# Performance work log

Measured on AMD Instinct MI355X. Metric: run time of the kernel, lower is better.

The kernel has to match this reference:

```python
import jax, jax.numpy as jnp
import numpy as np

N_NODES = 8192
N_EDGES = 16384
IN_CH = 32
HID = 64
OUT_CH = 2
EDGE_DIM = 4
N_LAYERS = 3
N_GRAPHS = 256
BN_EPS = 1e-5


def setup_inputs() -> dict:
    key = jax.random.key(0)
    ks = jax.random.split(key, 16)
    x = jax.random.normal(ks[0], (N_NODES, IN_CH), dtype=jnp.float32)
    edge_index = jax.random.randint(ks[1], (2, N_EDGES), 0, N_NODES, dtype=jnp.int32)
    edge_attr = jax.random.uniform(ks[2], (N_EDGES, EDGE_DIM), dtype=jnp.float32)
    batch = jnp.sort(jax.random.randint(ks[3], (N_NODES,), 0, N_GRAPHS, dtype=jnp.int32))
    s = 0.05
    params = {
        'lin_in_W': jax.random.normal(ks[4], (IN_CH, HID), jnp.float32) * s,
        'lin_in_b': jnp.zeros((HID,), jnp.float32),
        'edge_W': jax.random.normal(ks[5], (N_LAYERS, EDGE_DIM, HID * HID), jnp.float32) * s,
        'edge_b': jax.random.normal(ks[6], (N_LAYERS, HID * HID), jnp.float32) * s,
        'root_W': jax.random.normal(ks[7], (N_LAYERS, HID, HID), jnp.float32) * s,
        'conv_b': jnp.zeros((N_LAYERS, HID), jnp.float32),
        'bn_gamma': jnp.ones((N_LAYERS, HID), jnp.float32),
        'bn_beta': jnp.zeros((N_LAYERS, HID), jnp.float32),
        'bn_mean': jax.random.normal(ks[8], (N_LAYERS, HID), jnp.float32) * s,
        'bn_var': jax.random.uniform(ks[9], (N_LAYERS, HID), jnp.float32, 0.5, 1.5),
        'clf_W': jax.random.normal(ks[10], (HID, OUT_CH), jnp.float32) * s,
        'clf_b': jnp.zeros((OUT_CH,), jnp.float32),
    }
    return {'x': x, 'edge_index': edge_index, 'edge_attr': edge_attr, 'batch': batch, **params}


def reference(x, edge_index, edge_attr, batch, lin_in_W, lin_in_b, edge_W, edge_b,
              root_W, conv_b, bn_gamma, bn_beta, bn_mean, bn_var, clf_W, clf_b):
    # lin_in
    h = x @ lin_in_W + lin_in_b  # [N, H]
    src, dst = edge_index[0], edge_index[1]  # PyG: row0 = source j, row1 = target i
    for l in range(N_LAYERS):
        # edge network: per-edge weight matrix [E, H, H]
        W_e = (edge_attr @ edge_W[l] + edge_b[l]).reshape(N_EDGES, HID, HID)
        # message: gather x_j, per-edge matmul
        msg = jnp.einsum('eh,eho->eo', h[src], W_e)  # [E, H]
        # scatter-add aggregation at target nodes
        agg = jax.ops.segment_sum(msg, dst, num_segments=N_NODES)  # [N, H]
        # NNConv update: root transform + bias
        h = agg + h @ root_W[l] + conv_b[l]
        # BatchNorm1d (inference: running stats), then ReLU (dropout off in eval)
        h = (h - bn_mean[l]) * jax.lax.rsqrt(bn_var[l] + BN_EPS) * bn_gamma[l] + bn_beta[l]
        h = jax.nn.relu(h)
    # global_add_pool over graph ids
    pooled = jax.ops.segment_sum(h, batch, num_segments=N_GRAPHS)  # [G, H]
    return pooled @ clf_W + clf_b  # [G, OUT_CH]
```

## Files before the change

### kernel.cpp

```cpp
#include <hip/hip_runtime.h>

#define N_NODES 8192
#define N_EDGES 16384
#define IN_CH 32
#define HID 64
#define EDGE_DIM 4
#define N_LAYERS 3
#define N_GRAPHS 256
#define BN_EPS 1e-5f

#define NT 512
#define NPB 16
#define NBLK (N_NODES / NPB)
#define ECAP 96

__global__ void kzero(float4* __restrict__ p, int n4) {
    int i = blockIdx.x * blockDim.x + threadIdx.x;
    if (i < n4) p[i] = make_float4(0.f, 0.f, 0.f, 0.f);
}

__global__ __launch_bounds__(NT, 4) void k0(
        const float* __restrict__ x,
        const float* __restrict__ Win, const float* __restrict__ bin,
        const float* __restrict__ eW, const float* __restrict__ eB,
        const int* __restrict__ ei, const float* __restrict__ ea,
        float* __restrict__ hG, float* __restrict__ aggA,
        float* __restrict__ aggB, float* __restrict__ pooled,
        int* __restrict__ gbcnt, int2* __restrict__ gsd, float4* __restrict__ gea) {
    __shared__ float  Wis[IN_CH * HID];
    __shared__ float  xs[NPB * IN_CH];
    __shared__ float  hs[NPB * HID];
    __shared__ float  ys[NPB * 5 * HID];
    __shared__ int    cntE;
    __shared__ int2   eSL[ECAP];
    __shared__ float4 eEA[ECAP];

    const int t = threadIdx.x, b = blockIdx.x, node0 = b * NPB;
    const int c = t & 63, g = t >> 6;

    for (int i = t; i < NPB * HID; i += NT) aggB[node0 * HID + i] = 0.f;
    {
        int gi = b * NT + t;
        if (gi < N_GRAPHS * HID) pooled[gi] = 0.f;
    }
    if (t == 0) cntE = 0;
    for (int i = t; i < IN_CH * HID; i += NT) Wis[i] = Win[i];
    for (int i = t; i < NPB * IN_CH; i += NT) xs[i] = x[node0 * IN_CH + i];
    __syncthreads();

    {
        float bb = bin[c];
        float h0 = bb, h1 = bb;
        const float* x0 = xs + (2 * g + 0) * IN_CH;
        const float* x1 = xs + (2 * g + 1) * IN_CH;
#pragma unroll
        for (int k = 0; k < IN_CH; ++k) {
            float wk = Wis[k * HID + c];
            h0 += x0[k] * wk; h1 += x1[k] * wk;
        }
        hs[(2 * g + 0) * HID + c] = h0; hG[(node0 + 2 * g + 0) * HID + c] = h0;
        hs[(2 * g + 1) * HID + c] = h1; hG[(node0 + 2 * g + 1) * HID + c] = h1;
    }

    {
        float acc[2][5] = {};
#pragma unroll 4
        for (int k = 0; k < HID; ++k) {
            float w0 = eW[0 * 4096 + k * 64 + c];
            float w1 = eW[1 * 4096 + k * 64 + c];
            float w2 = eW[2 * 4096 + k * 64 + c];
            float w3 = eW[3 * 4096 + k * 64 + c];
            float w4 = eB[k * 64 + c];
            float a0 = hs[(2 * g + 0) * HID + k];
            float a1 = hs[(2 * g + 1) * HID + k];
            acc[0][0] += a0 * w0; acc[0][1] += a0 * w1; acc[0][2] += a0 * w2;
            acc[0][3] += a0 * w3; acc[0][4] += a0 * w4;
            acc[1][0] += a1 * w0; acc[1][1] += a1 * w1; acc[1][2] += a1 * w2;
            acc[1][3] += a1 * w3; acc[1][4] += a1 * w4;
        }
#pragma unroll
        for (int j = 0; j < 2; ++j)
#pragma unroll
            for (int d = 0; d < 5; ++d)
                ys[(2 * g + j) * (5 * HID) + d * HID + c] = acc[j][d];
    }

    for (int e = t; e < N_EDGES; e += NT) {
        int src = ei[e];
        if ((src >> 4) == b) {
            int slot = atomicAdd(&cntE, 1);
            if (slot < ECAP) {
                int2 sd = make_int2(src & 15, ei[N_EDGES + e]);
                float4 a4 = *(const float4*)(ea + 4 * (size_t)e);
                eSL[slot] = sd;           eEA[slot] = a4;
                gsd[b * ECAP + slot] = sd; gea[b * ECAP + slot] = a4;
            }
        }
    }
    __syncthreads();
    int cnt = min(cntE, ECAP);
    if (t == 0) gbcnt[b] = cnt;

    for (int e = g; e < cnt; e += 8) {
        int2 sd = eSL[e];
        float4 a = eEA[e];
        const float* yr = ys + sd.x * (5 * HID);
        float m = a.x * yr[c] + a.y * yr[HID + c] + a.z * yr[2 * HID + c] +
                  a.w * yr[3 * HID + c] + yr[4 * HID + c];
        atomicAdd(&aggA[sd.y * HID + c], m);
    }
}

template <int ZERO_IN, int LAST>
__global__ __launch_bounds__(NT, 4) void klayer(
        float* __restrict__ hG,
        float* __restrict__ aggIn, float* __restrict__ aggOut,
        const float* __restrict__ rootW, const float* __restrict__ conv_b,
        const float* __restrict__ gam, const float* __restrict__ bet,
        const float* __restrict__ mu, const float* __restrict__ var,
        const float* __restrict__ eW, const float* __restrict__ eB,
        const int* __restrict__ gbcnt, const int2* __restrict__ gsd,
        const float4* __restrict__ gea,
        const int* __restrict__ batch, float* __restrict__ pooled) {
    __shared__ float  Ws[HID * HID];
    __shared__ float  hsin[NPB * HID];
    __shared__ float  ys[NPB * 5 * HID];
    __shared__ int2   eSL[ECAP];
    __shared__ float4 eEA[ECAP];

    const int t = threadIdx.x, b = blockIdx.x, node0 = b * NPB;
    const int c = t & 63, g = t >> 6;

    int cnt = LAST ? 0 : min(gbcnt[b], ECAP);
    for (int i = t; i < HID * HID; i += NT) Ws[i] = rootW[i];
    for (int i = t; i < NPB * HID; i += NT) hsin[i] = hG[node0 * HID + i];
    if (!LAST) {
        for (int i = t; i < cnt; i += NT) { eSL[i] = gsd[b * ECAP + i]; eEA[i] = gea[b * ECAP + i]; }
    }
    __syncthreads();

    float scale = gam[c] * rsqrtf(var[c] + BN_EPS);
    float shift = bet[c] - mu[c] * scale;
    float cb = conv_b[c];

    float hnew[2];
#pragma unroll
    for (int j = 0; j < 2; ++j) {
        int ln = 2 * g + j, n = node0 + ln;
        float acc = 0.f;
        const float4* hv = (const float4*)(hsin + ln * HID);
#pragma unroll
        for (int k4 = 0; k4 < HID / 4; ++k4) {
            float4 h4 = hv[k4];
            acc += h4.x * Ws[(4 * k4 + 0) * 64 + c] + h4.y * Ws[(4 * k4 + 1) * 64 + c] +
                   h4.z * Ws[(4 * k4 + 2) * 64 + c] + h4.w * Ws[(4 * k4 + 3) * 64 + c];
        }
        float av = aggIn[n * HID + c];
        if (ZERO_IN) aggIn[n * HID + c] = 0.f;
        hnew[j] = fmaxf((av + acc + cb) * scale + shift, 0.f);
    }
    hsin[(2 * g + 0) * HID + c] = hnew[0];
    hsin[(2 * g + 1) * HID + c] = hnew[1];

    if (!LAST) {
        hG[(node0 + 2 * g + 0) * HID + c] = hnew[0];
        hG[(node0 + 2 * g + 1) * HID + c] = hnew[1];
        float acc[2][5] = {};
#pragma unroll 4
        for (int k = 0; k < HID; ++k) {
            float w0 = eW[0 * 4096 + k * 64 + c];
            float w1 = eW[1 * 4096 + k * 64 + c];
            float w2 = eW[2 * 4096 + k * 64 + c];
            float w3 = eW[3 * 4096 + k * 64 + c];
            float w4 = eB[k * 64 + c];
            float a0 = hsin[(2 * g + 0) * HID + k];
            float a1 = hsin[(2 * g + 1) * HID + k];
            acc[0][0] += a0 * w0; acc[0][1] += a0 * w1; acc[0][2] += a0 * w2;
            acc[0][3] += a0 * w3; acc[0][4] += a0 * w4;
            acc[1][0] += a1 * w0; acc[1][1] += a1 * w1; acc[1][2] += a1 * w2;
            acc[1][3] += a1 * w3; acc[1][4] += a1 * w4;
        }
#pragma unroll
        for (int j = 0; j < 2; ++j)
#pragma unroll
            for (int d = 0; d < 5; ++d)
                ys[(2 * g + j) * (5 * HID) + d * HID + c] = acc[j][d];
        __syncthreads();

        for (int e = g; e < cnt; e += 8) {
            int2 sd = eSL[e];
            float4 a = eEA[e];
            const float* yr = ys + sd.x * (5 * HID);
            float m = a.x * yr[c] + a.y * yr[HID + c] + a.z * yr[2 * HID + c] +
                      a.w * yr[3 * HID + c] + yr[4 * HID + c];
            atomicAdd(&aggOut[sd.y * HID + c], m);
        }
    } else {
        int n0 = node0 + 2 * g, n1 = n0 + 1;
        atomicAdd(&pooled[batch[n0] * HID + c], hnew[0]);
        atomicAdd(&pooled[batch[n1] * HID + c], hnew[1]);
    }
}

__global__ void kclf(const float* __restrict__ pooled,
                     const float* __restrict__ W,
                     const float* __restrict__ bb,
                     float* __restrict__ out) {
    int lane = threadIdx.x & 63;
    int gph = blockIdx.x * 4 + (threadIdx.x >> 6);
    float p = pooled[gph * HID + lane];
    float2 w = ((const float2*)W)[lane];
    float r0 = p * w.x, r1 = p * w.y;
#pragma unroll
    for (int off = 32; off; off >>= 1) {
        r0 += __shfl_xor(r0, off, 64);
        r1 += __shfl_xor(r1, off, 64);
    }
    if (lane == 0) {
        out[gph * 2 + 0] = r0 + bb[0];
        out[gph * 2 + 1] = r1 + bb[1];
    }
}

extern "C" void kernel_launch(void* const* d_in, const int* in_sizes, int n_in,
                              void* d_out, int out_size, void* d_ws, size_t ws_size,
                              hipStream_t stream) {
    const float* x         = (const float*)d_in[0];
    const int*   edge_index= (const int*)  d_in[1];
    const float* edge_attr = (const float*)d_in[2];
    const int*   batch     = (const int*)  d_in[3];
    const float* lin_in_W  = (const float*)d_in[4];
    const float* lin_in_b  = (const float*)d_in[5];
    const float* edge_W    = (const float*)d_in[6];
    const float* edge_b    = (const float*)d_in[7];
    const float* root_W    = (const float*)d_in[8];
    const float* conv_b    = (const float*)d_in[9];
    const float* bn_gamma  = (const float*)d_in[10];
    const float* bn_beta   = (const float*)d_in[11];
    const float* bn_mean   = (const float*)d_in[12];
    const float* bn_var    = (const float*)d_in[13];
    const float* clf_W     = (const float*)d_in[14];
    const float* clf_b     = (const float*)d_in[15];
    float* out = (float*)d_out;

    char* ws = (char*)d_ws;
    float*  aggA   = (float*) (ws);
    float*  aggB   = (float*) (ws + (size_t)2 * 1024 * 1024);
    float*  pooled = (float*) (ws + (size_t)4 * 1024 * 1024);
    int*    gbcnt  = (int*)   (ws + (size_t)4 * 1024 * 1024 + 65536);
    float*  hG     = (float*) (ws + (size_t)5 * 1024 * 1024);
    int2*   gsd    = (int2*)  (ws + (size_t)7 * 1024 * 1024);
    float4* gea    = (float4*)(ws + (size_t)7 * 1024 * 1024 + 512 * 1024);

    const int n4 = (2 * 1024 * 1024) / 16;
    kzero<<<(n4 + 255) / 256, 256, 0, stream>>>((float4*)aggA, n4);

    k0<<<NBLK, NT, 0, stream>>>(x, lin_in_W, lin_in_b, edge_W, edge_b,
                                edge_index, edge_attr, hG, aggA, aggB, pooled,
                                gbcnt, gsd, gea);

    klayer<1, 0><<<NBLK, NT, 0, stream>>>(
        hG, aggA, aggB, root_W, conv_b, bn_gamma, bn_beta, bn_mean, bn_var,
        edge_W + (size_t)1 * EDGE_DIM * HID * HID, edge_b + (size_t)1 * HID * HID,
        gbcnt, gsd, gea, batch, pooled);

    klayer<0, 0><<<NBLK, NT, 0, stream>>>(
        hG, aggB, aggA, root_W + (size_t)1 * HID * HID, conv_b + (size_t)1 * HID,
        bn_gamma + HID, bn_beta + HID, bn_mean + HID, bn_var + HID,
        edge_W + (size_t)2 * EDGE_DIM * HID * HID, edge_b + (size_t)2 * HID * HID,
        gbcnt, gsd, gea, batch, pooled);

    klayer<0, 1><<<NBLK, NT, 0, stream>>>(
        hG, aggA, aggB, root_W + (size_t)2 * HID * HID, conv_b + (size_t)2 * HID,
        bn_gamma + 2 * HID, bn_beta + 2 * HID, bn_mean + 2 * HID, bn_var + 2 * HID,
        edge_W, edge_b,
        gbcnt, gsd, gea, batch, pooled);

    kclf<<<N_GRAPHS / 4, 256, 0, stream>>>(pooled, clf_W, clf_b, out);
}
```

Before: 72.35 us.

## Pre-transpose weights to float4 layout, bin edges per node, fuse classifier into last layer

A prep kernel repacks lin_in, root and edge-network weights into a k4-interleaved float4 layout, zeroes the aggregation buffer and seeds the output with the classifier bias, replacing the zero kernel. Edges are binned per source node in registers-friendly per-node lists, so message values are computed directly from per-thread accumulators instead of staging a shared ys table and syncing. Root weights are read from global/L2 instead of being copied to shared memory, cutting LDS use and a barrier. The pooling plus classifier are fused into the last layer via wave reductions and atomics on the output, dropping the pooled buffer and kclf launch. Per-node cap of 20 edges could drop edges if a node has high out-degree.

```diff
diff --git a/kernel.cpp b/kernel.cpp
--- a/kernel.cpp
+++ b/kernel.cpp
@@ -12,102 +12,137 @@
 #define NT 512
 #define NPB 16
 #define NBLK (N_NODES / NPB)
-#define ECAP 96
-
-__global__ void kzero(float4* __restrict__ p, int n4) {
-    int i = blockIdx.x * blockDim.x + threadIdx.x;
-    if (i < n4) p[i] = make_float4(0.f, 0.f, 0.f, 0.f);
+#define NCAP 20
+
+#define WT_ROOT(l) (512 + (l) * 1024)
+#define WT_E(l) (3584 + (l) * 5120)
+#define WT_F4 18944
+
+__global__ __launch_bounds__(256) void kprep(
+        const float* __restrict__ Win, const float* __restrict__ rootW,
+        const float* __restrict__ eW, const float* __restrict__ eB,
+        const float* __restrict__ clf_b,
+        float4* __restrict__ WT4, float4* __restrict__ aggA4,
+        float* __restrict__ out) {
+    int i = blockIdx.x * 256 + threadIdx.x;
+    aggA4[i] = make_float4(0.f, 0.f, 0.f, 0.f);
+    if (i < N_GRAPHS * 2) out[i] = clf_b[i & 1];
+    if (i < WT_F4) {
+        const float* base;
+        int k4, c;
+        if (i < 512) {
+            k4 = i >> 6; c = i & 63; base = Win;
+        } else if (i < 3584) {
+            int oo = i - 512; int l = oo >> 10; int r = oo & 1023;
+            k4 = r >> 6; c = r & 63; base = rootW + l * 4096;
+        } else {
+            int oo = i - 3584; int l = oo / 5120; int r = oo % 5120;
+            int d = r >> 10; int rr = r & 1023;
+            k4 = rr >> 6; c = rr & 63;
+            base = (d < 4) ? (eW + (size_t)l * 16384 + d * 4096)
+                           : (eB + (size_t)l * 4096);
+        }
+        float4 v;
+        v.x = base[(k4 * 4 + 0) * 64 + c];
+        v.y = base[(k4 * 4 + 1) * 64 + c];
+        v.z = base[(k4 * 4 + 2) * 64 + c];
+        v.w = base[(k4 * 4 + 3) * 64 + c];
+        WT4[i] = v;
+    }
 }
 
 __global__ __launch_bounds__(NT, 4) void k0(
-        const float* __restrict__ x,
-        const float* __restrict__ Win, const float* __restrict__ bin,
-        const float* __restrict__ eW, const float* __restrict__ eB,
+        const float* __restrict__ x, const float* __restrict__ bin,
+        const float4* __restrict__ WT4,
         const int* __restrict__ ei, const float* __restrict__ ea,
-        float* __restrict__ hG, float* __restrict__ aggA,
-        float* __restrict__ aggB, float* __restrict__ pooled,
-        int* __restrict__ gbcnt, int2* __restrict__ gsd, float4* __restrict__ gea) {
-    __shared__ float  Wis[IN_CH * HID];
+        float* __restrict__ hG, float* __restrict__ aggA, float* __restrict__ aggB,
+        int* __restrict__ gcnt, int* __restrict__ gdst, float4* __restrict__ gea4) {
     __shared__ float  xs[NPB * IN_CH];
     __shared__ float  hs[NPB * HID];
-    __shared__ float  ys[NPB * 5 * HID];
-    __shared__ int    cntE;
-    __shared__ int2   eSL[ECAP];
-    __shared__ float4 eEA[ECAP];
+    __shared__ int    cntN[NPB];
+    __shared__ int    eDL[NPB * NCAP];
+    __shared__ float4 eEA[NPB * NCAP];
 
     const int t = threadIdx.x, b = blockIdx.x, node0 = b * NPB;
     const int c = t & 63, g = t >> 6;
 
-    for (int i = t; i < NPB * HID; i += NT) aggB[node0 * HID + i] = 0.f;
+    if (t < 256) ((float4*)(aggB + node0 * HID))[t] = make_float4(0.f, 0.f, 0.f, 0.f);
+    if (t < NPB) cntN[t] = 0;
     {
-        int gi = b * NT + t;
-        if (gi < N_GRAPHS * HID) pooled[gi] = 0.f;
-    }
-    if (t == 0) cntE = 0;
-    for (int i = t; i < IN_CH * HID; i += NT) Wis[i] = Win[i];
-    for (int i = t; i < NPB * IN_CH; i += NT) xs[i] = x[node0 * IN_CH + i];
+        int ln = 2 * g + (c >> 5);
+        xs[ln * IN_CH + (c & 31)] = x[(node0 + ln) * IN_CH + (c & 31)];
+    }
     __syncthreads();
+
+    const int4* src4 = (const int4*)ei;
+    for (int e4 = t; e4 < N_EDGES / 4; e4 += NT) {
+        int4 s4 = src4[e4];
+        int ss[4] = {s4.x, s4.y, s4.z, s4.w};
+#pragma unroll
+        for (int q = 0; q < 4; ++q) {
+            if ((ss[q] >> 4) == b) {
+                int local = ss[q] & 15;
+                int slot = atomicAdd(&cntN[local], 1);
+                if (slot < NCAP) {
+                    int e = e4 * 4 + q;
+                    int dst = ei[N_EDGES + e];
+                    float4 a4 = *(const float4*)(ea + 4 * (size_t)e);
+                    eDL[local * NCAP + slot] = dst;
+                    eEA[local * NCAP + slot] = a4;
+                    gdst[(node0 + local) * NCAP + slot] = dst;
+                    gea4[(node0 + local) * NCAP + slot] = a4;
+                }
+            }
+        }
+    }
 
     {
         float bb = bin[c];
         float h0 = bb, h1 = bb;
-        const float* x0 = xs + (2 * g + 0) * IN_CH;
-        const float* x1 = xs + (2 * g + 1) * IN_CH;
-#pragma unroll
-        for (int k = 0; k < IN_CH; ++k) {
-            float wk = Wis[k * HID + c];
-            h0 += x0[k] * wk; h1 += x1[k] * wk;
+        const float4* x0 = (const float4*)(xs + (2 * g + 0) * IN_CH);
+        const float4* x1 = (const float4*)(xs + (2 * g + 1) * IN_CH);
+#pragma unroll
+        for (int k4 = 0; k4 < IN_CH / 4; ++k4) {
+            float4 w = WT4[k4 * 64 + c];
+            float4 a = x0[k4], d = x1[k4];
+            h0 += a.x * w.x + a.y * w.y + a.z * w.z + a.w * w.w;
+            h1 += d.x * w.x + d.y * w.y + d.z * w.z + d.w * w.w;
         }
         hs[(2 * g + 0) * HID + c] = h0; hG[(node0 + 2 * g + 0) * HID + c] = h0;
         hs[(2 * g + 1) * HID + c] = h1; hG[(node0 + 2 * g + 1) * HID + c] = h1;
     }
 
+    float acc[2][5] = {};
     {
-        float acc[2][5] = {};
+        const float4* E = WT4 + WT_E(0);
+        const float4* h0v = (const float4*)(hs + (2 * g + 0) * HID);
+        const float4* h1v = (const float4*)(hs + (2 * g + 1) * HID);
 #pragma unroll 4
-        for (int k = 0; k < HID; ++k) {
-            float w0 = eW[0 * 4096 + k * 64 + c];
-            float w1 = eW[1 * 4096 + k * 64 + c];
-            float w2 = eW[2 * 4096 + k * 64 + c];
-            float w3 = eW[3 * 4096 + k * 64 + c];
-            float w4 = eB[k * 64 + c];
-            float a0 = hs[(2 * g + 0) * HID + k];
-            float a1 = hs[(2 * g + 1) * HID + k];
-            acc[0][0] += a0 * w0; acc[0][1] += a0 * w1; acc[0][2] += a0 * w2;
-            acc[0][3] += a0 * w3; acc[0][4] += a0 * w4;
-            acc[1][0] += a1 * w0; acc[1][1] += a1 * w1; acc[1][2] += a1 * w2;
-            acc[1][3] += a1 * w3; acc[1][4] += a1 * w4;
-        }
-#pragma unroll
-        for (int j = 0; j < 2; ++j)
-#pragma unroll
-            for (int d = 0; d < 5; ++d)
-                ys[(2 * g + j) * (5 * HID) + d * HID + c] = acc[j][d];
-    }
-
-    for (int e = t; e < N_EDGES; e += NT) {
-        int src = ei[e];
-        if ((src >> 4) == b) {
-            int slot = atomicAdd(&cntE, 1);
-            if (slot < ECAP) {
-                int2 sd = make_int2(src & 15, ei[N_EDGES + e]);
-                float4 a4 = *(const float4*)(ea + 4 * (size_t)e);
-                eSL[slot] = sd;           eEA[slot] = a4;
-                gsd[b * ECAP + slot] = sd; gea[b * ECAP + slot] = a4;
+        for (int k4 = 0; k4 < 16; ++k4) {
+            float4 a = h0v[k4], d = h1v[k4];
+#pragma unroll
+            for (int dd = 0; dd < 5; ++dd) {
+                float4 w = E[(dd * 16 + k4) * 64 + c];
+                acc[0][dd] += a.x * w.x + a.y * w.y + a.z * w.z + a.w * w.w;
+                acc[1][dd] += d.x * w.x + d.y * w.y + d.z * w.z + d.w * w.w;
             }
         }
     }
     __syncthreads();
-    int cnt = min(cntE, ECAP);
-    if (t == 0) gbcnt[b] = cnt;
-
-    for (int e = g; e < cnt; e += 8) {
-        int2 sd = eSL[e];
-        float4 a = eEA[e];
-        const float* yr = ys + sd.x * (5 * HID);
-        float m = a.x * yr[c] + a.y * yr[HID + c] + a.z * yr[2 * HID + c] +
-                  a.w * yr[3 * HID + c] + yr[4 * HID + c];
-        atomicAdd(&aggA[sd.y * HID + c], m);
+
+    if (t < NPB) gcnt[node0 + t] = min(cntN[t], NCAP);
+
+#pragma unroll
+    for (int j = 0; j < 2; ++j) {
+        int ln = 2 * g + j;
+        int cd = min(cntN[ln], NCAP);
+        for (int s = 0; s < cd; ++s) {
+            int dst = eDL[ln * NCAP + s];
+            float4 a = eEA[ln * NCAP + s];
+            float m = a.x * acc[j][0] + a.y * acc[j][1] + a.z * acc[j][2] +
+                      a.w * acc[j][3] + acc[j][4];
+            atomicAdd(&aggA[dst * HID + c], m);
+        }
     }
 }
 
@@ -115,45 +150,38 @@
 __global__ __launch_bounds__(NT, 4) void klayer(
         float* __restrict__ hG,
         float* __restrict__ aggIn, float* __restrict__ aggOut,
-        const float* __restrict__ rootW, const float* __restrict__ conv_b,
+        const float4* __restrict__ WT4, int lidx,
+        const float* __restrict__ conv_b,
         const float* __restrict__ gam, const float* __restrict__ bet,
         const float* __restrict__ mu, const float* __restrict__ var,
-        const float* __restrict__ eW, const float* __restrict__ eB,
-        const int* __restrict__ gbcnt, const int2* __restrict__ gsd,
-        const float4* __restrict__ gea,
-        const int* __restrict__ batch, float* __restrict__ pooled) {
-    __shared__ float  Ws[HID * HID];
-    __shared__ float  hsin[NPB * HID];
-    __shared__ float  ys[NPB * 5 * HID];
-    __shared__ int2   eSL[ECAP];
-    __shared__ float4 eEA[ECAP];
+        const int* __restrict__ gcnt, const int* __restrict__ gdst,
+        const float4* __restrict__ gea4,
+        const int* __restrict__ batch, const float* __restrict__ clfW,
+        float* __restrict__ out) {
+    __shared__ float hsin[NPB * HID];
 
     const int t = threadIdx.x, b = blockIdx.x, node0 = b * NPB;
     const int c = t & 63, g = t >> 6;
 
-    int cnt = LAST ? 0 : min(gbcnt[b], ECAP);
-    for (int i = t; i < HID * HID; i += NT) Ws[i] = rootW[i];
-    for (int i = t; i < NPB * HID; i += NT) hsin[i] = hG[node0 * HID + i];
-    if (!LAST) {
-        for (int i = t; i < cnt; i += NT) { eSL[i] = gsd[b * ECAP + i]; eEA[i] = gea[b * ECAP + i]; }
-    }
-    __syncthreads();
+    hsin[(2 * g + 0) * HID + c] = hG[(node0 + 2 * g + 0) * HID + c];
+    hsin[(2 * g + 1) * HID + c] = hG[(node0 + 2 * g + 1) * HID + c];
 
     float scale = gam[c] * rsqrtf(var[c] + BN_EPS);
     float shift = bet[c] - mu[c] * scale;
     float cb = conv_b[c];
 
+    const float4* R = WT4 + WT_ROOT(lidx);
     float hnew[2];
 #pragma unroll
     for (int j = 0; j < 2; ++j) {
         int ln = 2 * g + j, n = node0 + ln;
         float acc = 0.f;
         const float4* hv = (const float4*)(hsin + ln * HID);
-#pragma unroll
-        for (int k4 = 0; k4 < HID / 4; ++k4) {
+#pragma unroll 4
+        for (int k4 = 0; k4 < 16; ++k4) {
+            float4 w = R[k4 * 64 + c];
             float4 h4 = hv[k4];
-            acc += h4.x * Ws[(4 * k4 + 0) * 64 + c] + h4.y * Ws[(4 * k4 + 1) * 64 + c] +
-                   h4.z * Ws[(4 * k4 + 2) * 64 + c] + h4.w * Ws[(4 * k4 + 3) * 64 + c];
+            acc += h4.x * w.x + h4.y * w.y + h4.z * w.z + h4.w * w.w;
         }
         float av = aggIn[n * HID + c];
         if (ZERO_IN) aggIn[n * HID + c] = 0.f;
@@ -165,60 +193,51 @@
     if (!LAST) {
         hG[(node0 + 2 * g + 0) * HID + c] = hnew[0];
         hG[(node0 + 2 * g + 1) * HID + c] = hnew[1];
-        float acc[2][5] = {};
+
+        float acc2[2][5] = {};
+        const float4* E = WT4 + WT_E(lidx + 1);
+        const float4* h0v = (const float4*)(hsin + (2 * g + 0) * HID);
+        const float4* h1v = (const float4*)(hsin + (2 * g + 1) * HID);
 #pragma unroll 4
-        for (int k = 0; k < HID; ++k) {
-            float w0 = eW[0 * 4096 + k * 64 + c];
-            float w1 = eW[1 * 4096 + k * 64 + c];
-            float w2 = eW[2 * 4096 + k * 64 + c];
-            float w3 = eW[3 * 4096 + k * 64 + c];
-            float w4 = eB[k * 64 + c];
-            float a0 = hsin[(2 * g + 0) * HID + k];
-            float a1 = hsin[(2 * g + 1) * HID + k];
-            acc[0][0] += a0 * w0; acc[0][1] += a0 * w1; acc[0][2] += a0 * w2;
-            acc[0][3] += a0 * w3; acc[0][4] += a0 * w4;
-            acc[1][0] += a1 * w0; acc[1][1] += a1 * w1; acc[1][2] += a1 * w2;
-            acc[1][3] += a1 * w3; acc[1][4] += a1 * w4;
-        }
-#pragma unroll
-        for (int j = 0; j < 2; ++j)
-#pragma unroll
-            for (int d = 0; d < 5; ++d)
-                ys[(2 * g + j) * (5 * HID) + d * HID + c] = acc[j][d];
-        __syncthreads();
-
-        for (int e = g; e < cnt; e += 8) {
-            int2 sd = eSL[e];
-            float4 a = eEA[e];
-            const float* yr = ys + sd.x * (5 * HID);
-            float m = a.x * yr[c] + a.y * yr[HID + c] + a.z * yr[2 * HID + c] +
-                      a.w * yr[3 * HID + c] + yr[4 * HID + c];
-            atomicAdd(&aggOut[sd.y * HID + c], m);
+        for (int k4 = 0; k4 < 16; ++k4) {
+            float4 a = h0v[k4], d = h1v[k4];
+#pragma unroll
+            for (int dd = 0; dd < 5; ++dd) {
+                float4 w = E[(dd * 16 + k4) * 64 + c];
+                acc2[0][dd] += a.x * w.x + a.y * w.y + a.z * w.z + a.w * w.w;
+                acc2[1][dd] += d.x * w.x + d.y * w.y + d.z * w.z + d.w * w.w;
+            }
+        }
+#pragma unroll
+        for (int j = 0; j < 2; ++j) {
+            int n = node0 + 2 * g + j;
+            int cd = gcnt[n];
+            for (int s = 0; s < cd; ++s) {
+                int dst = gdst[n * NCAP + s];
+                float4 a = gea4[n * NCAP + s];
+                float m = a.x * acc2[j][0] + a.y * acc2[j][1] + a.z * acc2[j][2] +
+                          a.w * acc2[j][3] + acc2[j][4];
+                atomicAdd(&aggOut[dst * HID + c], m);
+            }
         }
     } else {
-        int n0 = node0 + 2 * g, n1 = n0 + 1;
-        atomicAdd(&pooled[batch[n0] * HID + c], hnew[0]);
-        atomicAdd(&pooled[batch[n1] * HID + c], hnew[1]);
-    }
-}
-
-__global__ void kclf(const float* __restrict__ pooled,
-                     const float* __restrict__ W,
-                     const float* __restrict__ bb,
-                     float* __restrict__ out) {
-    int lane = threadIdx.x & 63;
-    int gph = blockIdx.x * 4 + (threadIdx.x >> 6);
-    float p = pooled[gph * HID + lane];
-    float2 w = ((const float2*)W)[lane];
-    float r0 = p * w.x, r1 = p * w.y;
-#pragma unroll
-    for (int off = 32; off; off >>= 1) {
-        r0 += __shfl_xor(r0, off, 64);
-        r1 += __shfl_xor(r1, off, 64);
-    }
-    if (lane == 0) {
-        out[gph * 2 + 0] = r0 + bb[0];
-        out[gph * 2 + 1] = r1 + bb[1];
+        float2 w2 = ((const float2*)clfW)[c];
+#pragma unroll
+        for (int j = 0; j < 2; ++j) {
+            int n = node0 + 2 * g + j;
+            float v = hnew[j];
+            float r0 = v * w2.x, r1 = v * w2.y;
+#pragma unroll
+            for (int off = 32; off; off >>= 1) {
+                r0 += __shfl_xor(r0, off, 64);
+                r1 += __shfl_xor(r1, off, 64);
+            }
+            if (c == 0) {
+                int gg = batch[n];
+                atomicAdd(&out[gg * 2 + 0], r0);
+                atomicAdd(&out[gg * 2 + 1], r1);
+            }
+        }
     }
 }
 
@@ -244,37 +263,31 @@
     float* out = (float*)d_out;
 
     char* ws = (char*)d_ws;
-    float*  aggA   = (float*) (ws);
-    float*  aggB   = (float*) (ws + (size_t)2 * 1024 * 1024);
-    float*  pooled = (float*) (ws + (size_t)4 * 1024 * 1024);
-    int*    gbcnt  = (int*)   (ws + (size_t)4 * 1024 * 1024 + 65536);
-    float*  hG     = (float*) (ws + (size_t)5 * 1024 * 1024);
-    int2*   gsd    = (int2*)  (ws + (size_t)7 * 1024 * 1024);
-    float4* gea    = (float4*)(ws + (size_t)7 * 1024 * 1024 + 512 * 1024);
-
-    const int n4 = (2 * 1024 * 1024) / 16;
-    kzero<<<(n4 + 255) / 256, 256, 0, stream>>>((float4*)aggA, n4);
-
-    k0<<<NBLK, NT, 0, stream>>>(x, lin_in_W, lin_in_b, edge_W, edge_b,
-                                edge_index, edge_attr, hG, aggA, aggB, pooled,
-                                gbcnt, gsd, gea);
+    float*  aggA = (float*) (ws);
+    float*  aggB = (float*) (ws + (size_t)2 * 1024 * 1024);
+    float*  hG   = (float*) (ws + (size_t)4 * 1024 * 1024);
+    int*    gcnt = (int*)   (ws + (size_t)6 * 1024 * 1024);
+    int*    gdst = (int*)   (ws + (size_t)6 * 1024 * 1024 + 65536);
+    float4* gea4 = (float4*)(ws + (size_t)7 * 1024 * 1024);
+    float4* WT4  = (float4*)(ws + (size_t)10 * 1024 * 1024);
+
+    kprep<<<512, 256, 0, stream>>>(lin_in_W, root_W, edge_W, edge_b, clf_b,
+                                   WT4, (float4*)aggA, out);
+
+    k0<<<NBLK, NT, 0, stream>>>(x, lin_in_b, WT4, edge_index, edge_attr,
+                                hG, aggA, aggB, gcnt, gdst, gea4);
 
     klayer<1, 0><<<NBLK, NT, 0, stream>>>(
-        hG, aggA, aggB, root_W, conv_b, bn_gamma, bn_beta, bn_mean, bn_var,
-        edge_W + (size_t)1 * EDGE_DIM * HID * HID, edge_b + (size_t)1 * HID * HID,
-        gbcnt, gsd, gea, batch, pooled);
+        hG, aggA, aggB, WT4, 0, conv_b, bn_gamma, bn_beta, bn_mean, bn_var,
+        gcnt, gdst, gea4, batch, clf_W, out);
 
     klayer<0, 0><<<NBLK, NT, 0, stream>>>(
-        hG, aggB, aggA, root_W + (size_t)1 * HID * HID, conv_b + (size_t)1 * HID,
+        hG, aggB, aggA, WT4, 1, conv_b + HID,
         bn_gamma + HID, bn_beta + HID, bn_mean + HID, bn_var + HID,
-        edge_W + (size_t)2 * EDGE_DIM * HID * HID, edge_b + (size_t)2 * HID * HID,
-        gbcnt, gsd, gea, batch, pooled);
+        gcnt, gdst, gea4, batch, clf_W, out);
 
     klayer<0, 1><<<NBLK, NT, 0, stream>>>(
-        hG, aggA, aggB, root_W + (size_t)2 * HID * HID, conv_b + (size_t)2 * HID,
+        hG, aggA, aggB, WT4, 2, conv_b + 2 * HID,
         bn_gamma + 2 * HID, bn_beta + 2 * HID, bn_mean + 2 * HID, bn_var + 2 * HID,
-        edge_W, edge_b,
-        gbcnt, gsd, gea, batch, pooled);
-
-    kclf<<<N_GRAPHS / 4, 256, 0, stream>>>(pooled, clf_W, clf_b, out);
-}
+        gcnt, gdst, gea4, batch, clf_W, out);
+}
```

New measurement: 119.1 us. +64.6%, slower.

## Replace scatter-atomic aggregation with dst-bucketed gather of per-node edge projections

Applied to the files above, without the earlier changes.

Edges are now bucketed by destination node (up to 24 per node) instead of by source block. Per-node projections y = h·[W_e0..3, b] are written to global memory, and the next layer gathers them by source to build the message sum without atomics. This removes the zeroing kernel and the global atomicAdd scatter. In exchange it adds an extra global write and a random gather of 5 values per edge, and it silently drops edges beyond the per-node cap.

```diff
diff --git a/kernel.cpp b/kernel.cpp
--- a/kernel.cpp
+++ b/kernel.cpp
@@ -12,41 +12,51 @@
 #define NT 512
 #define NPB 16
 #define NBLK (N_NODES / NPB)
-#define ECAP 96
-
-__global__ void kzero(float4* __restrict__ p, int n4) {
-    int i = blockIdx.x * blockDim.x + threadIdx.x;
-    if (i < n4) p[i] = make_float4(0.f, 0.f, 0.f, 0.f);
-}
+#define NCAP 24
 
 __global__ __launch_bounds__(NT, 4) void k0(
         const float* __restrict__ x,
         const float* __restrict__ Win, const float* __restrict__ bin,
         const float* __restrict__ eW, const float* __restrict__ eB,
         const int* __restrict__ ei, const float* __restrict__ ea,
-        float* __restrict__ hG, float* __restrict__ aggA,
-        float* __restrict__ aggB, float* __restrict__ pooled,
-        int* __restrict__ gbcnt, int2* __restrict__ gsd, float4* __restrict__ gea) {
-    __shared__ float  Wis[IN_CH * HID];
-    __shared__ float  xs[NPB * IN_CH];
-    __shared__ float  hs[NPB * HID];
-    __shared__ float  ys[NPB * 5 * HID];
-    __shared__ int    cntE;
-    __shared__ int2   eSL[ECAP];
-    __shared__ float4 eEA[ECAP];
+        float* __restrict__ hG, float4* __restrict__ y4, float* __restrict__ yb,
+        float* __restrict__ pooled,
+        int* __restrict__ gcnt, int* __restrict__ gsrc, float4* __restrict__ gea4) {
+    __shared__ float Wis[IN_CH * HID];
+    __shared__ float xs[NPB * IN_CH];
+    __shared__ float hs[NPB * HID];
+    __shared__ int   cntN[NPB];
 
     const int t = threadIdx.x, b = blockIdx.x, node0 = b * NPB;
     const int c = t & 63, g = t >> 6;
 
-    for (int i = t; i < NPB * HID; i += NT) aggB[node0 * HID + i] = 0.f;
     {
         int gi = b * NT + t;
         if (gi < N_GRAPHS * HID) pooled[gi] = 0.f;
     }
-    if (t == 0) cntE = 0;
+    if (t < NPB) cntN[t] = 0;
     for (int i = t; i < IN_CH * HID; i += NT) Wis[i] = Win[i];
     for (int i = t; i < NPB * IN_CH; i += NT) xs[i] = x[node0 * IN_CH + i];
     __syncthreads();
+
+    const int4* dst4 = (const int4*)(ei + N_EDGES);
+    for (int e4 = t; e4 < N_EDGES / 4; e4 += NT) {
+        int4 d4 = dst4[e4];
+        int ds[4] = {d4.x, d4.y, d4.z, d4.w};
+#pragma unroll
+        for (int q = 0; q < 4; ++q) {
+            int local = ds[q] - node0;
+            if ((unsigned)local < NPB) {
+                int slot = atomicAdd(&cntN[local], 1);
+                if (slot < NCAP) {
+                    int e = e4 * 4 + q;
+                    gsrc[(node0 + local) * NCAP + slot] = ei[e];
+                    gea4[(node0 + local) * NCAP + slot] =
+                        *(const float4*)(ea + 4 * (size_t)e);
+                }
+            }
+        }
+    }
 
     {
         float bb = bin[c];
@@ -79,64 +89,38 @@
             acc[1][3] += a1 * w3; acc[1][4] += a1 * w4;
         }
 #pragma unroll
-        for (int j = 0; j < 2; ++j)
-#pragma unroll
-            for (int d = 0; d < 5; ++d)
-                ys[(2 * g + j) * (5 * HID) + d * HID + c] = acc[j][d];
-    }
-
-    for (int e = t; e < N_EDGES; e += NT) {
-        int src = ei[e];
-        if ((src >> 4) == b) {
-            int slot = atomicAdd(&cntE, 1);
-            if (slot < ECAP) {
-                int2 sd = make_int2(src & 15, ei[N_EDGES + e]);
-                float4 a4 = *(const float4*)(ea + 4 * (size_t)e);
-                eSL[slot] = sd;           eEA[slot] = a4;
-                gsd[b * ECAP + slot] = sd; gea[b * ECAP + slot] = a4;
-            }
-        }
-    }
+        for (int j = 0; j < 2; ++j) {
+            size_t n = node0 + 2 * g + j;
+            y4[n * HID + c] = make_float4(acc[j][0], acc[j][1], acc[j][2], acc[j][3]);
+            yb[n * HID + c] = acc[j][4];
+        }
+    }
+
     __syncthreads();
-    int cnt = min(cntE, ECAP);
-    if (t == 0) gbcnt[b] = cnt;
-
-    for (int e = g; e < cnt; e += 8) {
-        int2 sd = eSL[e];
-        float4 a = eEA[e];
-        const float* yr = ys + sd.x * (5 * HID);
-        float m = a.x * yr[c] + a.y * yr[HID + c] + a.z * yr[2 * HID + c] +
-                  a.w * yr[3 * HID + c] + yr[4 * HID + c];
-        atomicAdd(&aggA[sd.y * HID + c], m);
-    }
-}
-
-template <int ZERO_IN, int LAST>
-__global__ __launch_bounds__(NT, 4) void klayer(
+    if (t < NPB) gcnt[node0 + t] = min(cntN[t], NCAP);
+}
+
+template <int LAST>
+__global__ __launch_bounds__(NT, 4) void kupd(
         float* __restrict__ hG,
-        float* __restrict__ aggIn, float* __restrict__ aggOut,
+        const float4* __restrict__ ycur4, const float* __restrict__ ycurb,
+        float4* __restrict__ ynxt4, float* __restrict__ ynxtb,
         const float* __restrict__ rootW, const float* __restrict__ conv_b,
         const float* __restrict__ gam, const float* __restrict__ bet,
         const float* __restrict__ mu, const float* __restrict__ var,
         const float* __restrict__ eW, const float* __restrict__ eB,
-        const int* __restrict__ gbcnt, const int2* __restrict__ gsd,
-        const float4* __restrict__ gea,
+        const int* __restrict__ gcnt, const int* __restrict__ gsrc,
+        const float4* __restrict__ gea4,
         const int* __restrict__ batch, float* __restrict__ pooled) {
-    __shared__ float  Ws[HID * HID];
-    __shared__ float  hsin[NPB * HID];
-    __shared__ float  ys[NPB * 5 * HID];
-    __shared__ int2   eSL[ECAP];
-    __shared__ float4 eEA[ECAP];
+    __shared__ float Ws[HID * HID];
+    __shared__ float hsin[NPB * HID];
 
     const int t = threadIdx.x, b = blockIdx.x, node0 = b * NPB;
     const int c = t & 63, g = t >> 6;
 
-    int cnt = LAST ? 0 : min(gbcnt[b], ECAP);
     for (int i = t; i < HID * HID; i += NT) Ws[i] = rootW[i];
-    for (int i = t; i < NPB * HID; i += NT) hsin[i] = hG[node0 * HID + i];
-    if (!LAST) {
-        for (int i = t; i < cnt; i += NT) { eSL[i] = gsd[b * ECAP + i]; eEA[i] = gea[b * ECAP + i]; }
-    }
+    hsin[(2 * g + 0) * HID + c] = hG[(node0 + 2 * g + 0) * HID + c];
+    hsin[(2 * g + 1) * HID + c] = hG[(node0 + 2 * g + 1) * HID + c];
     __syncthreads();
 
     float scale = gam[c] * rsqrtf(var[c] + BN_EPS);
@@ -147,6 +131,15 @@
 #pragma unroll
     for (int j = 0; j < 2; ++j) {
         int ln = 2 * g + j, n = node0 + ln;
+        float m = 0.f;
+        int cd = gcnt[n];
+        for (int s = 0; s < cd; ++s) {
+            int src = gsrc[n * NCAP + s];
+            float4 a = gea4[n * NCAP + s];
+            float4 yv = ycur4[(size_t)src * HID + c];
+            m += a.x * yv.x + a.y * yv.y + a.z * yv.z + a.w * yv.w +
+                 ycurb[(size_t)src * HID + c];
+        }
         float acc = 0.f;
         const float4* hv = (const float4*)(hsin + ln * HID);
 #pragma unroll
@@ -155,9 +148,7 @@
             acc += h4.x * Ws[(4 * k4 + 0) * 64 + c] + h4.y * Ws[(4 * k4 + 1) * 64 + c] +
                    h4.z * Ws[(4 * k4 + 2) * 64 + c] + h4.w * Ws[(4 * k4 + 3) * 64 + c];
         }
-        float av = aggIn[n * HID + c];
-        if (ZERO_IN) aggIn[n * HID + c] = 0.f;
-        hnew[j] = fmaxf((av + acc + cb) * scale + shift, 0.f);
+        hnew[j] = fmaxf((m + acc + cb) * scale + shift, 0.f);
     }
     hsin[(2 * g + 0) * HID + c] = hnew[0];
     hsin[(2 * g + 1) * HID + c] = hnew[1];
@@ -181,19 +172,10 @@
             acc[1][3] += a1 * w3; acc[1][4] += a1 * w4;
         }
 #pragma unroll
-        for (int j = 0; j < 2; ++j)
-#pragma unroll
-            for (int d = 0; d < 5; ++d)
-                ys[(2 * g + j) * (5 * HID) + d * HID + c] = acc[j][d];
-        __syncthreads();
-
-        for (int e = g; e < cnt; e += 8) {
-            int2 sd = eSL[e];
-            float4 a = eEA[e];
-            const float* yr = ys + sd.x * (5 * HID);
-            float m = a.x * yr[c] + a.y * yr[HID + c] + a.z * yr[2 * HID + c] +
-                      a.w * yr[3 * HID + c] + yr[4 * HID + c];
-            atomicAdd(&aggOut[sd.y * HID + c], m);
+        for (int j = 0; j < 2; ++j) {
+            size_t n = node0 + 2 * g + j;
+            ynxt4[n * HID + c] = make_float4(acc[j][0], acc[j][1], acc[j][2], acc[j][3]);
+            ynxtb[n * HID + c] = acc[j][4];
         }
     } else {
         int n0 = node0 + 2 * g, n1 = n0 + 1;
@@ -244,37 +226,39 @@
     float* out = (float*)d_out;
 
     char* ws = (char*)d_ws;
-    float*  aggA   = (float*) (ws);
-    float*  aggB   = (float*) (ws + (size_t)2 * 1024 * 1024);
-    float*  pooled = (float*) (ws + (size_t)4 * 1024 * 1024);
-    int*    gbcnt  = (int*)   (ws + (size_t)4 * 1024 * 1024 + 65536);
-    float*  hG     = (float*) (ws + (size_t)5 * 1024 * 1024);
-    int2*   gsd    = (int2*)  (ws + (size_t)7 * 1024 * 1024);
-    float4* gea    = (float4*)(ws + (size_t)7 * 1024 * 1024 + 512 * 1024);
-
-    const int n4 = (2 * 1024 * 1024) / 16;
-    kzero<<<(n4 + 255) / 256, 256, 0, stream>>>((float4*)aggA, n4);
+    float4* yA4    = (float4*)(ws);
+    float4* yB4    = (float4*)(ws + (size_t) 8 * 1024 * 1024);
+    float*  ybA    = (float*) (ws + (size_t)16 * 1024 * 1024);
+    float*  ybB    = (float*) (ws + (size_t)18 * 1024 * 1024);
+    float*  pooled = (float*) (ws + (size_t)20 * 1024 * 1024);
+    int*    gcnt   = (int*)   (ws + (size_t)20 * 1024 * 1024 + 65536);
+    float*  hG     = (float*) (ws + (size_t)21 * 1024 * 1024);
+    int*    gsrc   = (int*)   (ws + (size_t)23 * 1024 * 1024);
+    float4* gea4   = (float4*)(ws + (size_t)24 * 1024 * 1024);
 
     k0<<<NBLK, NT, 0, stream>>>(x, lin_in_W, lin_in_b, edge_W, edge_b,
-                                edge_index, edge_attr, hG, aggA, aggB, pooled,
-                                gbcnt, gsd, gea);
-
-    klayer<1, 0><<<NBLK, NT, 0, stream>>>(
-        hG, aggA, aggB, root_W, conv_b, bn_gamma, bn_beta, bn_mean, bn_var,
+                                edge_index, edge_attr, hG, yA4, ybA, pooled,
+                                gcnt, gsrc, gea4);
+
+    kupd<0><<<NBLK, NT, 0, stream>>>(
+        hG, yA4, ybA, yB4, ybB,
+        root_W, conv_b, bn_gamma, bn_beta, bn_mean, bn_var,
         edge_W + (size_t)1 * EDGE_DIM * HID * HID, edge_b + (size_t)1 * HID * HID,
-        gbcnt, gsd, gea, batch, pooled);
-
-    klayer<0, 0><<<NBLK, NT, 0, stream>>>(
-        hG, aggB, aggA, root_W + (size_t)1 * HID * HID, conv_b + (size_t)1 * HID,
+        gcnt, gsrc, gea4, batch, pooled);
+
+    kupd<0><<<NBLK, NT, 0, stream>>>(
+        hG, yB4, ybB, yA4, ybA,
+        root_W + (size_t)1 * HID * HID, conv_b + (size_t)1 * HID,
         bn_gamma + HID, bn_beta + HID, bn_mean + HID, bn_var + HID,
         edge_W + (size_t)2 * EDGE_DIM * HID * HID, edge_b + (size_t)2 * HID * HID,
-        gbcnt, gsd, gea, batch, pooled);
-
-    klayer<0, 1><<<NBLK, NT, 0, stream>>>(
-        hG, aggA, aggB, root_W + (size_t)2 * HID * HID, conv_b + (size_t)2 * HID,
+        gcnt, gsrc, gea4, batch, pooled);
+
+    kupd<1><<<NBLK, NT, 0, stream>>>(
+        hG, yA4, ybA, yB4, ybB,
+        root_W + (size_t)2 * HID * HID, conv_b + (size_t)2 * HID,
         bn_gamma + 2 * HID, bn_beta + 2 * HID, bn_mean + 2 * HID, bn_var + 2 * HID,
         edge_W, edge_b,
-        gbcnt, gsd, gea, batch, pooled);
+        gcnt, gsrc, gea4, batch, pooled);
 
     kclf<<<N_GRAPHS / 4, 256, 0, stream>>>(pooled, clf_W, clf_b, out);
 }
```

Result: slower. 100.0 us (+38.3%).
